# Optimization experiments

Measured on AMD Instinct MI355X. Metric: run time of the kernel, lower is better.

## Reference

```python
import jax, jax.numpy as jnp
import numpy as np

EPS = 0.01
N_NODES = 12288
D_PLUS_1 = 65  # 64-dim position + 1 mass
N_EDGES = 262144


def setup_inputs() -> dict:
    key = jax.random.key(0)
    k1, k2 = jax.random.split(key)
    z = jax.random.normal(k1, (N_NODES, D_PLUS_1), dtype=jnp.float32)
    l = jnp.ones((1,), dtype=jnp.float32)  # learnable gravity exponent, init 1.0
    edge_label_index = jax.random.randint(k2, (2, N_EDGES), 0, N_NODES, dtype=jnp.int64)
    return {"z": z, "l": l, "edge_label_index": edge_label_index}


def _multiclass_probs(logits_uv, logits_vu):
    s_uv = jax.nn.sigmoid(logits_uv)
    s_vu = jax.nn.sigmoid(logits_vu)
    p_nb = (1.0 - s_uv) * (1.0 - s_vu)
    p_pu = s_uv * (1.0 - s_vu)
    p_pb = s_uv * s_vu
    p_nu = (1.0 - s_uv) * s_vu
    return jnp.stack([p_nb, p_pu, p_pb, p_nu], axis=1)  # [E, 4]


def reference(z, l, edge_label_index):
    # Full pairwise log-squared-distance logits (as the original decode_all does).
    m = z[:, -1]          # [N] masses
    r = z[:, :-1]         # [N, d] positions
    norm = jnp.sum(r * r, axis=1, keepdims=True)          # [N, 1]
    r2 = norm - 2.0 * (r @ r.T) + norm.T                  # [N, N] squared distances
    logr2 = jnp.log(r2 + EPS)                             # CLAMP is None -> no clamp
    # adj[i, j] = m_j - l * log(||r_i - r_j||^2 + EPS)
    adj = m[None, :] - l * logr2                          # [N, N]
    u = edge_label_index[0]
    v = edge_label_index[1]
    logit_uv = adj[u, v]
    logit_vu = adj[v, u]
    return _multiclass_probs(logit_uv, logit_vu)          # sigmoid=True -> probs [E, 4]
```

## Files before the change

### kernel.cpp

```cpp
#include <hip/hip_runtime.h>


constexpr int kNodes = 12288;
constexpr int kD     = 64;
constexpr int kRow   = 65;
constexpr int kEdges = 262144;
constexpr float kEps = 0.01f;

__global__ __launch_bounds__(256) void edge_kernel(
    const float* __restrict__ z,
    const float* __restrict__ lptr,
    const int*   __restrict__ eidx,
    float4*      __restrict__ out)
{
    const float l = lptr[0];
    const int tid = blockIdx.x * blockDim.x + threadIdx.x;
    const int sub = tid & 15;
    const int estride = (gridDim.x * blockDim.x) >> 4;

    for (int e = tid >> 4; e < kEdges; e += estride) {
        const int u = eidx[e];
        const int v = eidx[kEdges + e];
        const float* zu = z + (long)u * kRow + sub * 4;
        const float* zv = z + (long)v * kRow + sub * 4;

        float p = 0.f;
#pragma unroll
        for (int j = 0; j < 4; ++j) {
            const float d = zu[j] - zv[j];
            p = fmaf(d, d, p);
        }
        p += __shfl_xor(p, 1);
        p += __shfl_xor(p, 2);
        p += __shfl_xor(p, 4);
        p += __shfl_xor(p, 8);

        if (sub == 0) {
            const float logd     = __logf(p + kEps);
            const float logit_uv = z[(long)v * kRow + kD] - l * logd;
            const float logit_vu = z[(long)u * kRow + kD] - l * logd;
            const float suv = 1.f / (1.f + __expf(-logit_uv));
            const float svu = 1.f / (1.f + __expf(-logit_vu));
            out[e] = make_float4((1.f - suv) * (1.f - svu),
                                 suv         * (1.f - svu),
                                 suv         * svu,
                                 (1.f - suv) * svu);
        }
    }
}

extern "C" void kernel_launch(void* const* d_in, const int* in_sizes, int n_in,
                              void* d_out, int out_size, void* d_ws, size_t ws_size,
                              hipStream_t stream) {
    const float* z    = (const float*)d_in[0];
    const float* lptr = (const float*)d_in[1];
    const int*   eidx = (const int*)d_in[2];
    float4*      out  = (float4*)d_out;

    edge_kernel<<<dim3(4096), dim3(256), 0, stream>>>(z, lptr, eidx, out);
}
```

Baseline: 72.92 us.

## Repack node rows to 16-byte aligned stride and use float4 gathers

Adds a repack kernel that copies z into a workspace buffer with row stride 68 instead of 65, so each 16-lane group can load its four position values with one aligned float4 load per node. The edge kernel also drops its grid-stride loop and launches one 16-thread group per edge. The point is fewer, wider gather loads in exchange for an extra kernel launch and a roughly 3 MB copy each call.

Result: slower. 78.74 us (+8.0%).

```diff
diff --git a/kernel.cpp b/kernel.cpp
--- a/kernel.cpp
+++ b/kernel.cpp
@@ -3,49 +3,66 @@
 
 constexpr int kNodes = 12288;
 constexpr int kD     = 64;
-constexpr int kRow   = 65;
+constexpr int kRowIn = 65;
+constexpr int kRowP  = 68;
 constexpr int kEdges = 262144;
 constexpr float kEps = 0.01f;
 
+__global__ __launch_bounds__(256) void repack_kernel(
+    const float* __restrict__ z, float* __restrict__ zp)
+{
+    const int i = blockIdx.x * 256 + threadIdx.x;
+    if (i < kNodes * kRowIn) {
+        const int row = i / kRowIn;
+        const int col = i - row * kRowIn;
+        zp[row * kRowP + col] = z[i];
+    }
+}
+
 __global__ __launch_bounds__(256) void edge_kernel(
-    const float* __restrict__ z,
+    const float* __restrict__ zp,
     const float* __restrict__ lptr,
     const int*   __restrict__ eidx,
     float4*      __restrict__ out)
 {
+    const int tid = blockIdx.x * 256 + threadIdx.x;
+    const int e   = tid >> 4;
+    const int sub = tid & 15;
+
+    const int u = eidx[e];
+    const int v = eidx[kEdges + e];
     const float l = lptr[0];
-    const int tid = blockIdx.x * blockDim.x + threadIdx.x;
-    const int sub = tid & 15;
-    const int estride = (gridDim.x * blockDim.x) >> 4;
 
-    for (int e = tid >> 4; e < kEdges; e += estride) {
-        const int u = eidx[e];
-        const int v = eidx[kEdges + e];
-        const float* zu = z + (long)u * kRow + sub * 4;
-        const float* zv = z + (long)v * kRow + sub * 4;
+    const float* ru = zp + u * kRowP;
+    const float* rv = zp + v * kRowP;
 
-        float p = 0.f;
-#pragma unroll
-        for (int j = 0; j < 4; ++j) {
-            const float d = zu[j] - zv[j];
-            p = fmaf(d, d, p);
-        }
-        p += __shfl_xor(p, 1);
-        p += __shfl_xor(p, 2);
-        p += __shfl_xor(p, 4);
-        p += __shfl_xor(p, 8);
+    const float mu = ru[kD];
+    const float mv = rv[kD];
 
-        if (sub == 0) {
-            const float logd     = __logf(p + kEps);
-            const float logit_uv = z[(long)v * kRow + kD] - l * logd;
-            const float logit_vu = z[(long)u * kRow + kD] - l * logd;
-            const float suv = 1.f / (1.f + __expf(-logit_uv));
-            const float svu = 1.f / (1.f + __expf(-logit_vu));
-            out[e] = make_float4((1.f - suv) * (1.f - svu),
-                                 suv         * (1.f - svu),
-                                 suv         * svu,
-                                 (1.f - suv) * svu);
-        }
+    const float4 a = *(const float4*)(ru + sub * 4);
+    const float4 b = *(const float4*)(rv + sub * 4);
+
+    float p;
+    {
+        const float dx = a.x - b.x, dy = a.y - b.y;
+        const float dz = a.z - b.z, dw = a.w - b.w;
+        p = fmaf(dx, dx, fmaf(dy, dy, fmaf(dz, dz, dw * dw)));
+    }
+    p += __shfl_xor(p, 1);
+    p += __shfl_xor(p, 2);
+    p += __shfl_xor(p, 4);
+    p += __shfl_xor(p, 8);
+
+    if (sub == 0) {
+        const float logd = __logf(p + kEps);
+        const float luv  = mv - l * logd;
+        const float lvu  = mu - l * logd;
+        const float suv  = 1.f / (1.f + __expf(-luv));
+        const float svu  = 1.f / (1.f + __expf(-lvu));
+        out[e] = make_float4((1.f - suv) * (1.f - svu),
+                             suv         * (1.f - svu),
+                             suv         * svu,
+                             (1.f - suv) * svu);
     }
 }
 
@@ -55,7 +72,11 @@
     const float* z    = (const float*)d_in[0];
     const float* lptr = (const float*)d_in[1];
     const int*   eidx = (const int*)d_in[2];
+    float*       zp   = (float*)d_ws;
     float4*      out  = (float4*)d_out;
 
-    edge_kernel<<<dim3(4096), dim3(256), 0, stream>>>(z, lptr, eidx, out);
+    const int n_elems = kNodes * kRowIn;
+    repack_kernel<<<dim3((n_elems + 255) / 256), dim3(256), 0, stream>>>(z, zp);
+
+    edge_kernel<<<dim3(kEdges * 16 / 256), dim3(256), 0, stream>>>(zp, lptr, eidx, out);
 }
```
